# Kernel tuning notes

Measured on AMD Instinct MI355X. Metric: run time of the kernel, lower is better.

Reference implementation:

```python
import jax, jax.numpy as jnp
import numpy as np

B = 4; E_PER = 100_000; E = B * E_PER
N_NODES = 50_000; N_REL = 500; D = 64; D_LG = 256
K_PER_VI = 20; S_VI = E // K_PER_VI          # 20000 sorted vi segments
S_VJ_PER = 5_000; S_VJ = B * S_VJ_PER        # 20000 unsorted vj segments
N_MEM = 131_072
INTERACT = ((0, 3), (0, 2, 3), (0, 4), (0, 2, 4), (1, 3), (1, 2, 3), (1, 4), (1, 2, 4))


def _build_edges():
    rng = np.random.default_rng(0)
    idx_vi = np.repeat(np.arange(S_VI), K_PER_VI)          # sorted segment ids
    gpb = S_VI // B
    eg = idx_vi // gpb                                     # sorted by eg_idx too
    vi = rng.integers(0, N_NODES, S_VI)[idx_vi]
    idx_vj = np.empty(E, dtype=np.int64)
    for b in range(B):
        loc = np.concatenate([np.arange(S_VJ_PER), rng.integers(0, S_VJ_PER, E_PER - S_VJ_PER)])
        rng.shuffle(loc)
        idx_vj[b * E_PER:(b + 1) * E_PER] = b * S_VJ_PER + loc  # every group non-empty
    vj = rng.integers(0, N_NODES, S_VJ)[idx_vj]            # consistent (eg, vj) per group
    rel = rng.integers(0, N_REL, E)
    e2vi = rng.integers(0, N_MEM, E)
    e2vj = rng.integers(0, N_MEM, E)
    return np.stack([eg, vi, vj, rel, idx_vi, idx_vj, e2vi, e2vj], axis=1).astype(np.int32)


def setup_inputs() -> dict:
    key = jax.random.key(0)
    ks = jax.random.split(key, 10)
    return {
        "node_attention": jax.random.uniform(ks[0], (B, N_NODES), jnp.float32),
        "scanned_edges": jnp.asarray(_build_edges()),
        "edges_y": jax.random.uniform(ks[1], (E,), jnp.float32),
        "hidden_uncon": jax.random.normal(ks[2], (1, N_NODES, D_LG), jnp.float32),
        "hidden_con": jax.random.normal(ks[3], (N_MEM, D), jnp.float32),
        "Wc": jax.random.normal(ks[4], (D, D), jnp.float32) / np.sqrt(D).astype(np.float32),
        "bc": jnp.zeros((D,), jnp.float32),
        "Wu": jax.random.normal(ks[5], (D_LG, D), jnp.float32) / np.sqrt(D_LG).astype(np.float32),
        "bu": jnp.zeros((D,), jnp.float32),
        "rel_table": jax.random.normal(ks[6], (N_REL, D), jnp.float32) * 0.05,
        "ws": jax.random.normal(ks[7], (len(INTERACT), D), jnp.float32) / np.sqrt(float(len(INTERACT))).astype(np.float32) if False else jax.random.normal(ks[7], (len(INTERACT), D), jnp.float32) * (1.0 / np.sqrt(len(INTERACT)).astype(np.float32)),
        "fb": jnp.zeros((D,), jnp.float32),
        "out_w": jax.random.normal(ks[8], (D,), jnp.float32),
        "out_b": jnp.zeros((D,), jnp.float32),
        "n_vi_segments": S_VI,
        "n_vj_segments": S_VJ,
    }


def reference(node_attention, scanned_edges, edges_y, hidden_uncon, hidden_con,
              Wc, bc, Wu, bu, rel_table, ws, fb, out_w, out_b,
              n_vi_segments, n_vj_segments):
    eg, vi, vj, rel = (scanned_edges[:, i] for i in range(4))
    idx_vi, idx_vj, e2vi, e2vj = (scanned_edges[:, i] for i in range(4, 8))
    # projections (proj_con / proj_uncon, tanh Dense)
    hc = jnp.tanh(hidden_con @ Wc + bc)          # [N_MEM, D]
    hu = jnp.tanh(hidden_uncon @ Wu + bu)[0]     # [n_nodes, D]; batch_size==1 path of Node2Edge
    # Node2Edge gathers
    feats = (hc[e2vi], hu[vi], rel_table[rel], hc[e2vj], hu[vj])  # each [E, D]
    # F layer: weighted sum of elementwise interaction products
    out = fb
    for k, idxs in enumerate(INTERACT):
        x = feats[idxs[0]]
        for i in idxs[1:]:
            x = x * feats[i]
        out = out + x * ws[k]
    out = jax.nn.relu(out) * out_w + out_b
    logits = jnp.sum(out, axis=1)                # [E]
    # NeighborSoftmax at 'vi' (sorted segment softmax)
    m = jax.ops.segment_max(logits, idx_vi, num_segments=n_vi_segments)
    ex = jnp.exp(logits - m[idx_vi])
    den = jax.ops.segment_sum(ex, idx_vi, num_segments=n_vi_segments)
    transition = ex / den[idx_vi]
    # attention flow: gather source attention, weight, aggregate at vj
    trans_att = transition * node_attention[eg, vi] * edges_y
    aggr = jax.ops.segment_sum(trans_att, idx_vj, num_segments=n_vj_segments)
    b_g = jax.ops.segment_max(eg, idx_vj, num_segments=n_vj_segments)
    vj_g = jax.ops.segment_max(vj, idx_vj, num_segments=n_vj_segments)
    new_node_attention = jnp.zeros_like(node_attention).at[b_g, vj_g].add(aggr)
    return new_node_attention
```

## Files before the change

### kernel.cpp

```cpp
#include <hip/hip_runtime.h>
#include <hip/hip_bf16.h>

#define D 64
#define KPER 20

typedef __attribute__((ext_vector_type(8))) short short8;
typedef __attribute__((ext_vector_type(4))) float floatx4;

__device__ __forceinline__ short f2bf(float x) {
    __hip_bfloat16 h = __float2bfloat16(x);
    return *reinterpret_cast<short*>(&h);
}

template<typename T> __device__ __forceinline__ T to_T(float x);
template<> __device__ __forceinline__ float to_T<float>(float x) { return x; }
template<> __device__ __forceinline__ __hip_bfloat16 to_T<__hip_bfloat16>(float x) { return __float2bfloat16(x); }

template<typename T> __device__ __forceinline__ float to_f(T x);
template<> __device__ __forceinline__ float to_f<float>(float x) { return x; }
template<> __device__ __forceinline__ float to_f<__hip_bfloat16>(__hip_bfloat16 x) { return __bfloat162float(x); }

template<int K, typename T>
__global__ __launch_bounds__(256) void proj_mfma(const float* __restrict__ h,
        const float* __restrict__ W, const float* __restrict__ b,
        T* __restrict__ out, int ntiles) {
    constexpr int PAD = 8;
    __shared__ short Wl[64 * (K + PAD)];
    int tid = threadIdx.x;
    for (int i = tid; i < K * 64; i += 256) {
        int k = i >> 6, n = i & 63;
        Wl[n * (K + PAD) + k] = f2bf(W[i]);
    }
    __syncthreads();
    int lane = tid & 63;
    int m = lane & 15, quad = lane >> 4;
    int w = tid >> 6;
    for (int rt = blockIdx.x * 4 + w; rt < ntiles; rt += gridDim.x * 4) {
        floatx4 acc[4];
        #pragma unroll
        for (int ct = 0; ct < 4; ++ct) acc[ct] = floatx4{0.f, 0.f, 0.f, 0.f};
        const float* hrow = h + (size_t)(rt * 16 + m) * K + quad * 8;
        #pragma unroll
        for (int kt = 0; kt < K / 32; ++kt) {
            floatx4 a0 = *(const floatx4*)(hrow + kt * 32);
            floatx4 a1 = *(const floatx4*)(hrow + kt * 32 + 4);
            short8 af;
            af[0] = f2bf(a0[0]); af[1] = f2bf(a0[1]);
            af[2] = f2bf(a0[2]); af[3] = f2bf(a0[3]);
            af[4] = f2bf(a1[0]); af[5] = f2bf(a1[1]);
            af[6] = f2bf(a1[2]); af[7] = f2bf(a1[3]);
            #pragma unroll
            for (int ct = 0; ct < 4; ++ct) {
                short8 bf = *(const short8*)(&Wl[(ct * 16 + m) * (K + PAD) + kt * 32 + quad * 8]);
                acc[ct] = __builtin_amdgcn_mfma_f32_16x16x32_bf16(af, bf, acc[ct], 0, 0, 0);
            }
        }
        #pragma unroll
        for (int ct = 0; ct < 4; ++ct) {
            int col = ct * 16 + m;
            float bv = b[col];
            #pragma unroll
            for (int reg = 0; reg < 4; ++reg) {
                int row = rt * 16 + quad * 4 + reg;
                out[(size_t)row * 64 + col] = to_T<T>(tanhf(acc[ct][reg] + bv));
            }
        }
    }
}

template<typename T>
__global__ __launch_bounds__(256) void edge_kernel(
        const float* __restrict__ natt, const int* __restrict__ edges,
        const float* __restrict__ ey, const T* __restrict__ hc,
        const T* __restrict__ hu, const float* __restrict__ relt,
        const float* __restrict__ wsm, const float* __restrict__ fb,
        const float* __restrict__ outw, float* __restrict__ out, int N) {
    int lane = threadIdx.x & 63;
    int s = blockIdx.x * 4 + (threadIdx.x >> 6);
    long base = (long)s * KPER;
    const int* e0 = edges + base * 8;
    int eg = e0[0], vi = e0[1];
    float f1 = to_f<T>(hu[(size_t)vi * D + lane]);
    float na = natt[(size_t)eg * N + vi];
    float w0 = wsm[0 * D + lane], w1 = wsm[1 * D + lane];
    float w2 = wsm[2 * D + lane], w3 = wsm[3 * D + lane];
    float w4 = wsm[4 * D + lane], w5 = wsm[5 * D + lane];
    float w6 = wsm[6 * D + lane], w7 = wsm[7 * D + lane];
    float fbv = fb[lane], owv = outw[lane];
    float myl = -INFINITY;
    int myvj = 0;
    #pragma unroll 4
    for (int e = 0; e < KPER; ++e) {
        const int* er = edges + (base + e) * 8;
        int vj = er[2], rel = er[3], evi = er[6], evj = er[7];
        float F0 = to_f<T>(hc[(size_t)evi * D + lane]);
        float F2 = relt[(size_t)rel * D + lane];
        float F3 = to_f<T>(hc[(size_t)evj * D + lane]);
        float F4 = to_f<T>(hu[(size_t)vj * D + lane]);
        float t1 = fmaf(F2, w1, w0);
        float t2 = fmaf(F2, w5, w4);
        float t3 = fmaf(F2, w3, w2);
        float t4 = fmaf(F2, w7, w6);
        float u = fmaf(F0, t1, f1 * t2);
        float v = fmaf(F0, t3, f1 * t4);
        float o = fmaf(F3, u, fmaf(F4, v, fbv));
        o = fmaxf(o, 0.0f) * owv;
        #pragma unroll
        for (int mm = 1; mm < 64; mm <<= 1) o += __shfl_xor(o, mm);
        if (lane == e) { myl = o; myvj = vj; }
    }
    float mx = myl;
    #pragma unroll
    for (int mm = 1; mm < 64; mm <<= 1) mx = fmaxf(mx, __shfl_xor(mx, mm));
    float ex = __expf(myl - mx);
    float den = ex;
    #pragma unroll
    for (int mm = 1; mm < 64; mm <<= 1) den += __shfl_xor(den, mm);
    if (lane < KPER) {
        float t = (ex / den) * na * ey[base + lane];
        atomicAdd(out + (size_t)eg * N + myvj, t);
    }
}

extern "C" void kernel_launch(void* const* d_in, const int* in_sizes, int n_in,
                              void* d_out, int out_size, void* d_ws, size_t ws_size,
                              hipStream_t stream) {
    const float* natt = (const float*)d_in[0];
    const int*   edges = (const int*)d_in[1];
    const float* ey   = (const float*)d_in[2];
    const float* hun  = (const float*)d_in[3];
    const float* hcon = (const float*)d_in[4];
    const float* Wc   = (const float*)d_in[5];
    const float* bc   = (const float*)d_in[6];
    const float* Wu   = (const float*)d_in[7];
    const float* bu   = (const float*)d_in[8];
    const float* relt = (const float*)d_in[9];
    const float* wsm  = (const float*)d_in[10];
    const float* fb   = (const float*)d_in[11];
    const float* outw = (const float*)d_in[12];
    float* out = (float*)d_out;

    int E    = in_sizes[2];
    int S    = E / KPER;
    int nmem = in_sizes[4] / D;
    int N    = in_sizes[3] / 256;

    hipMemsetAsync(d_out, 0, (size_t)out_size * sizeof(float), stream);

    int t64  = nmem / 16;
    int t256 = N / 16;

    size_t need_f32 = ((size_t)nmem + (size_t)N) * D * sizeof(float);
    if (ws_size >= need_f32) {
        float* hc = (float*)d_ws;
        float* hu = hc + (size_t)nmem * D;
        proj_mfma<64, float><<<(t64 + 3) / 4, 256, 0, stream>>>(hcon, Wc, bc, hc, t64);
        proj_mfma<256, float><<<(t256 + 3) / 4, 256, 0, stream>>>(hun, Wu, bu, hu, t256);
        edge_kernel<float><<<S / 4, 256, 0, stream>>>(natt, edges, ey, hc, hu,
                                                      relt, wsm, fb, outw, out, N);
    } else {
        __hip_bfloat16* hc = (__hip_bfloat16*)d_ws;
        __hip_bfloat16* hu = hc + (size_t)nmem * D;
        proj_mfma<64, __hip_bfloat16><<<(t64 + 3) / 4, 256, 0, stream>>>(hcon, Wc, bc, hc, t64);
        proj_mfma<256, __hip_bfloat16><<<(t256 + 3) / 4, 256, 0, stream>>>(hun, Wu, bu, hu, t256);
        edge_kernel<__hip_bfloat16><<<S / 4, 256, 0, stream>>>(natt, edges, ey, hc, hu,
                                                               relt, wsm, fb, outw, out, N);
    }
}
```

Before: 233.0 us.

## Fuse projections into one persistent kernel, register-resident weights, fast tanh, DPP reductions

The two projection launches become one kernel with a fixed grid of persistent blocks: the first half projects hidden_con and the second half projects hidden_uncon, with each wave handling half of the output columns. Weight fragments are held in registers instead of being staged through LDS, which removes the shared-memory fill and the barrier. tanhf is replaced by an exp/rcp approximation. The edge kernel's shuffle-based wave reductions become DPP plus readlane sequences. Together these aim to cut launch overhead, LDS traffic and reduction latency, at the cost of more register pressure and slightly lower tanh accuracy.

```diff
diff --git a/kernel.cpp b/kernel.cpp
--- a/kernel.cpp
+++ b/kernel.cpp
@@ -20,28 +20,61 @@
 template<> __device__ __forceinline__ float to_f<float>(float x) { return x; }
 template<> __device__ __forceinline__ float to_f<__hip_bfloat16>(__hip_bfloat16 x) { return __bfloat162float(x); }
 
-template<int K, typename T>
-__global__ __launch_bounds__(256) void proj_mfma(const float* __restrict__ h,
+__device__ __forceinline__ float fast_tanh(float x) {
+    float xc = fminf(fmaxf(x, -15.f), 15.f);
+    float e = __expf(2.f * xc);
+    return 1.f - 2.f * __builtin_amdgcn_rcpf(1.f + e);
+}
+
+template<int CTRL>
+__device__ __forceinline__ float dpp_add(float x) {
+    int t = __builtin_amdgcn_update_dpp(0, __float_as_int(x), CTRL, 0xf, 0xf, true);
+    return x + __int_as_float(t);
+}
+template<int CTRL>
+__device__ __forceinline__ float dpp_max(float x) {
+    int xi = __float_as_int(x);
+    int t = __builtin_amdgcn_update_dpp(xi, xi, CTRL, 0xf, 0xf, false);
+    return fmaxf(x, __int_as_float(t));
+}
+__device__ __forceinline__ float wave_sum_b(float x) {
+    x = dpp_add<0x111>(x); x = dpp_add<0x112>(x);
+    x = dpp_add<0x114>(x); x = dpp_add<0x118>(x);
+    x = dpp_add<0x142>(x); x = dpp_add<0x143>(x);
+    return __int_as_float(__builtin_amdgcn_readlane(__float_as_int(x), 63));
+}
+__device__ __forceinline__ float wave_max_b(float x) {
+    x = dpp_max<0x111>(x); x = dpp_max<0x112>(x);
+    x = dpp_max<0x114>(x); x = dpp_max<0x118>(x);
+    x = dpp_max<0x142>(x); x = dpp_max<0x143>(x);
+    return __int_as_float(__builtin_amdgcn_readlane(__float_as_int(x), 63));
+}
+
+template<int K, int CTN, typename T>
+__device__ __forceinline__ void proj_body(const float* __restrict__ h,
         const float* __restrict__ W, const float* __restrict__ b,
-        T* __restrict__ out, int ntiles) {
-    constexpr int PAD = 8;
-    __shared__ short Wl[64 * (K + PAD)];
-    int tid = threadIdx.x;
-    for (int i = tid; i < K * 64; i += 256) {
-        int k = i >> 6, n = i & 63;
-        Wl[n * (K + PAD) + k] = f2bf(W[i]);
-    }
-    __syncthreads();
-    int lane = tid & 63;
+        T* __restrict__ out, int ct0, int rt0, int rtstride, int ntiles) {
+    constexpr int KT = K / 32;
+    int lane = threadIdx.x & 63;
     int m = lane & 15, quad = lane >> 4;
-    int w = tid >> 6;
-    for (int rt = blockIdx.x * 4 + w; rt < ntiles; rt += gridDim.x * 4) {
-        floatx4 acc[4];
-        #pragma unroll
-        for (int ct = 0; ct < 4; ++ct) acc[ct] = floatx4{0.f, 0.f, 0.f, 0.f};
+    short8 bfr[CTN][KT];
+    #pragma unroll
+    for (int ct = 0; ct < CTN; ++ct)
+        #pragma unroll
+        for (int kt = 0; kt < KT; ++kt)
+            #pragma unroll
+            for (int j = 0; j < 8; ++j)
+                bfr[ct][kt][j] = f2bf(W[(size_t)(kt * 32 + quad * 8 + j) * 64 + (ct0 + ct) * 16 + m]);
+    float bv[CTN];
+    #pragma unroll
+    for (int ct = 0; ct < CTN; ++ct) bv[ct] = b[(ct0 + ct) * 16 + m];
+    for (int rt = rt0; rt < ntiles; rt += rtstride) {
+        floatx4 acc[CTN];
+        #pragma unroll
+        for (int ct = 0; ct < CTN; ++ct) acc[ct] = floatx4{0.f, 0.f, 0.f, 0.f};
         const float* hrow = h + (size_t)(rt * 16 + m) * K + quad * 8;
         #pragma unroll
-        for (int kt = 0; kt < K / 32; ++kt) {
+        for (int kt = 0; kt < KT; ++kt) {
             floatx4 a0 = *(const floatx4*)(hrow + kt * 32);
             floatx4 a1 = *(const floatx4*)(hrow + kt * 32 + 4);
             short8 af;
@@ -50,21 +83,35 @@
             af[4] = f2bf(a1[0]); af[5] = f2bf(a1[1]);
             af[6] = f2bf(a1[2]); af[7] = f2bf(a1[3]);
             #pragma unroll
-            for (int ct = 0; ct < 4; ++ct) {
-                short8 bf = *(const short8*)(&Wl[(ct * 16 + m) * (K + PAD) + kt * 32 + quad * 8]);
-                acc[ct] = __builtin_amdgcn_mfma_f32_16x16x32_bf16(af, bf, acc[ct], 0, 0, 0);
-            }
+            for (int ct = 0; ct < CTN; ++ct)
+                acc[ct] = __builtin_amdgcn_mfma_f32_16x16x32_bf16(af, bfr[ct][kt], acc[ct], 0, 0, 0);
         }
         #pragma unroll
-        for (int ct = 0; ct < 4; ++ct) {
-            int col = ct * 16 + m;
-            float bv = b[col];
+        for (int ct = 0; ct < CTN; ++ct) {
+            int col = (ct0 + ct) * 16 + m;
             #pragma unroll
             for (int reg = 0; reg < 4; ++reg) {
                 int row = rt * 16 + quad * 4 + reg;
-                out[(size_t)row * 64 + col] = to_T<T>(tanhf(acc[ct][reg] + bv));
+                out[(size_t)row * 64 + col] = to_T<T>(fast_tanh(acc[ct][reg] + bv[ct]));
             }
         }
+    }
+}
+
+template<typename T>
+__global__ __launch_bounds__(256) void proj_fused(
+        const float* __restrict__ hcon, const float* __restrict__ Wc, const float* __restrict__ bc,
+        const float* __restrict__ hun, const float* __restrict__ Wu, const float* __restrict__ bu,
+        T* __restrict__ hc, T* __restrict__ hu, int t64, int t256, int g64) {
+    int w = threadIdx.x >> 6;
+    if ((int)blockIdx.x < g64) {
+        int wid = blockIdx.x * 4 + w;
+        proj_body<64, 4, T>(hcon, Wc, bc, hc, 0, wid, g64 * 4, t64);
+    } else {
+        int g256 = gridDim.x - g64;
+        int wid = (blockIdx.x - g64) * 4 + w;
+        int half = wid & 1;
+        proj_body<256, 2, T>(hun, Wu, bu, hu, half * 2, wid >> 1, (g256 * 4) >> 1, t256);
     }
 }
 
@@ -105,17 +152,14 @@
         float v = fmaf(F0, t3, f1 * t4);
         float o = fmaf(F3, u, fmaf(F4, v, fbv));
         o = fmaxf(o, 0.0f) * owv;
-        #pragma unroll
-        for (int mm = 1; mm < 64; mm <<= 1) o += __shfl_xor(o, mm);
-        if (lane == e) { myl = o; myvj = vj; }
-    }
-    float mx = myl;
-    #pragma unroll
-    for (int mm = 1; mm < 64; mm <<= 1) mx = fmaxf(mx, __shfl_xor(mx, mm));
+        float tot = wave_sum_b(o);
+        bool mine = (lane == e);
+        myl = mine ? tot : myl;
+        myvj = mine ? vj : myvj;
+    }
+    float mx = wave_max_b(myl);
     float ex = __expf(myl - mx);
-    float den = ex;
-    #pragma unroll
-    for (int mm = 1; mm < 64; mm <<= 1) den += __shfl_xor(den, mm);
+    float den = wave_sum_b(ex);
     if (lane < KPER) {
         float t = (ex / den) * na * ey[base + lane];
         atomicAdd(out + (size_t)eg * N + myvj, t);
@@ -149,20 +193,21 @@
 
     int t64  = nmem / 16;
     int t256 = N / 16;
+    int g64  = 512, g256 = 512;
 
     size_t need_f32 = ((size_t)nmem + (size_t)N) * D * sizeof(float);
     if (ws_size >= need_f32) {
         float* hc = (float*)d_ws;
         float* hu = hc + (size_t)nmem * D;
-        proj_mfma<64, float><<<(t64 + 3) / 4, 256, 0, stream>>>(hcon, Wc, bc, hc, t64);
-        proj_mfma<256, float><<<(t256 + 3) / 4, 256, 0, stream>>>(hun, Wu, bu, hu, t256);
+        proj_fused<float><<<g64 + g256, 256, 0, stream>>>(hcon, Wc, bc, hun, Wu, bu,
+                                                          hc, hu, t64, t256, g64);
         edge_kernel<float><<<S / 4, 256, 0, stream>>>(natt, edges, ey, hc, hu,
                                                       relt, wsm, fb, outw, out, N);
     } else {
         __hip_bfloat16* hc = (__hip_bfloat16*)d_ws;
         __hip_bfloat16* hu = hc + (size_t)nmem * D;
-        proj_mfma<64, __hip_bfloat16><<<(t64 + 3) / 4, 256, 0, stream>>>(hcon, Wc, bc, hc, t64);
-        proj_mfma<256, __hip_bfloat16><<<(t256 + 3) / 4, 256, 0, stream>>>(hun, Wu, bu, hu, t256);
+        proj_fused<__hip_bfloat16><<<g64 + g256, 256, 0, stream>>>(hcon, Wc, bc, hun, Wu, bu,
+                                                                   hc, hu, t64, t256, g64);
         edge_kernel<__hip_bfloat16><<<S / 4, 256, 0, stream>>>(natt, edges, ey, hc, hu,
                                                                relt, wsm, fb, outw, out, N);
     }
```

After: 224.7 us. 3.6% less time.
